# Kernel tuning notes

Hardware: AMD Instinct MI355X
Metric: run time of the kernel (lower is better)

The kernel has to match this reference:

```python
import jax, jax.numpy as jnp
import numpy as np

H, N, CH = 256, 64, 1  # heads/features, diagonal state size, channels


def setup_inputs() -> dict:
    key = jax.random.key(0)
    k1, k2, k3 = jax.random.split(key, 3)
    # |A| in (0.5, 0.999) so exp(dtA * l) decays for large l (matches rho*w construction)
    A_abslog = jnp.log(jax.random.uniform(k1, (H, N), dtype=jnp.float32,
                                          minval=0.5, maxval=0.999))
    A_phase = jax.random.uniform(k2, (H, N), dtype=jnp.float32,
                                 minval=-np.pi, maxval=np.pi)
    # C stored as real view of complex (channels, H, N, 2), like torch.view_as_real
    C = jax.random.normal(k3, (CH, H, N, 2), dtype=jnp.float32)
    return {"A_abslog": A_abslog, "A_phase": A_phase, "C": C, "L": 4096}


def reference(A_abslog, A_phase, C, L):
    # A_eigvals = exp(abslog + i*phase), copies=1 so repeat is identity
    A = jnp.exp(A_abslog + 1j * A_phase)            # (H, N) complex64
    dtA = jnp.log(A)                                 # (H, N)
    Cc = C[..., 0] + 1j * C[..., 1]                  # (CH, H, N)
    Cc = Cc * (A - 1.0) / dtA                        # (CH, H, N)
    t = jnp.arange(L, dtype=jnp.float32)             # (L,)
    K = jnp.exp(dtA[:, :, None] * t)                 # (H, N, L) Vandermonde
    K = jnp.einsum('chn,hnl->chl', Cc, K)            # (CH, H, L)
    return 2.0 * K.real
```

## Files before the change

kernel.cpp:

```cpp
#include <hip/hip_runtime.h>
#include <math.h>


typedef _Float16 f16x8 __attribute__((ext_vector_type(8)));
typedef unsigned short u16x8 __attribute__((ext_vector_type(8)));
typedef unsigned int   u32x4 __attribute__((ext_vector_type(4)));
typedef float          f32x4 __attribute__((ext_vector_type(4)));

constexpr int H = 256;
constexpr int N = 64;
constexpr int L = 4096;
constexpr int STRIDE = 76;

__global__ __launch_bounds__(256)
void sskdiag_kernel(const float* __restrict__ A_abslog,
                    const float* __restrict__ A_phase,
                    const float* __restrict__ C,
                    float* __restrict__ out)
{
    __shared__ float4   s_t1[N];
    __shared__ float4   s_t2[N];
    __shared__ unsigned s_G[64 * STRIDE];
    __shared__ unsigned s_M[64 * STRIDE];

    const int h   = blockIdx.x;
    const int tid = threadIdx.x;

    if (tid < N) {
        const int n = tid;
        const float al = A_abslog[h * N + n];
        const float ph = A_phase [h * N + n];
        const double md = (double)ph * 0.15915494309189535;
        const float phrev = (float)(md - floor(md));
        const float sp = __builtin_amdgcn_sinf(phrev);
        const float cp = __builtin_amdgcn_cosf(phrev);
        const float m  = __expf(al);
        const float Ar = m * cp, Ai = m * sp;
        const float nr = Ar - 1.0f, ni = Ai;
        const float inv = 1.0f / (al * al + ph * ph);
        const float gr = (nr * al + ni * ph) * inv;
        const float gi = (ni * al - nr * ph) * inv;
        const float cre = C[(h * N + n) * 2 + 0];
        const float cim = C[(h * N + n) * 2 + 1];
        const float Cr = 2.0f * (cre * gr - cim * gi);
        const float Ci = 2.0f * (cre * gi + cim * gr);
        const double m64 = 64.0 * md;
        const float f64a = (float)(m64 - floor(m64));
        const float mg64 = __expf(64.0f * al);
        s_t1[n] = make_float4(al, phrev, Ar, Ai);
        s_t2[n] = make_float4(mg64 * __builtin_amdgcn_cosf(f64a),
                              mg64 * __builtin_amdgcn_sinf(f64a), Cr, Ci);
    }
    __syncthreads();

    {
        const int n = tid & 63, q = tid >> 6;
        const float4 t1 = s_t1[n];
        const float4 t2 = s_t2[n];
        const float al = t1.x, phrev = t1.y;
        const float Ar = t1.z, Ai = t1.w;
        const float Ur = t2.x, Ui = t2.y;
        const float b0 = (float)(16 * q);
        float tg = phrev * b0;  tg -= floorf(tg);
        const float gmag = __expf(al * b0);
        float gre = gmag * __builtin_amdgcn_cosf(tg);
        float gim = gmag * __builtin_amdgcn_sinf(tg);
        const float a64 = (float)(1024 * q);
        float tm = phrev * a64;  tm -= floorf(tm);
        const float umag = __expf(al * a64);
        const float ure = umag * __builtin_amdgcn_cosf(tm);
        const float uim = umag * __builtin_amdgcn_sinf(tm);
        float mre = t2.z * ure - t2.w * uim;
        float mim = t2.z * uim + t2.w * ure;

        #pragma unroll
        for (int k = 0; k < 16; ++k) {
            const int row = 16 * q + k;
            union { _Float16 hh[2]; unsigned u; } pg, pm;
            pg.hh[0] = (_Float16)gre;  pg.hh[1] = (_Float16)(-gim);
            pm.hh[0] = (_Float16)mre;  pm.hh[1] = (_Float16)mim;
            s_G[row * STRIDE + n] = pg.u;
            s_M[row * STRIDE + n] = pm.u;
            const float ngr = gre * Ar - gim * Ai;
            gim = gre * Ai + gim * Ar;  gre = ngr;
            const float nmr = mre * Ur - mim * Ui;
            mim = mre * Ui + mim * Ur;  mre = nmr;
        }
    }
    __syncthreads();

    const int w    = tid >> 6;
    const int lane = tid & 63;
    const int e    = lane & 15;
    const int kg   = lane >> 4;

    f16x8 fGr[2][4], fGi[2][4], fMr[2], fMi[2];

    #pragma unroll
    for (int s = 0; s < 2; ++s) {
        #pragma unroll
        for (int tb = 0; tb < 4; ++tb) {
            const unsigned* p = &s_G[(tb * 16 + e) * STRIDE + 32 * s + 8 * kg];
            const u32x4 v0 = *reinterpret_cast<const u32x4*>(p);
            const u32x4 v1 = *reinterpret_cast<const u32x4*>(p + 4);
            u16x8 rr, ii;
            #pragma unroll
            for (int k = 0; k < 4; ++k) {
                rr[k]     = (unsigned short)(v0[k] & 0xffffu);
                ii[k]     = (unsigned short)(v0[k] >> 16);
                rr[k + 4] = (unsigned short)(v1[k] & 0xffffu);
                ii[k + 4] = (unsigned short)(v1[k] >> 16);
            }
            fGr[s][tb] = __builtin_bit_cast(f16x8, rr);
            fGi[s][tb] = __builtin_bit_cast(f16x8, ii);
        }
        {
            const unsigned* p = &s_M[(w * 16 + e) * STRIDE + 32 * s + 8 * kg];
            const u32x4 v0 = *reinterpret_cast<const u32x4*>(p);
            const u32x4 v1 = *reinterpret_cast<const u32x4*>(p + 4);
            u16x8 rr, ii;
            #pragma unroll
            for (int k = 0; k < 4; ++k) {
                rr[k]     = (unsigned short)(v0[k] & 0xffffu);
                ii[k]     = (unsigned short)(v0[k] >> 16);
                rr[k + 4] = (unsigned short)(v1[k] & 0xffffu);
                ii[k + 4] = (unsigned short)(v1[k] >> 16);
            }
            fMr[s] = __builtin_bit_cast(f16x8, rr);
            fMi[s] = __builtin_bit_cast(f16x8, ii);
        }
    }

    #pragma unroll
    for (int tb = 0; tb < 4; ++tb) {
        f32x4 acc = {0.f, 0.f, 0.f, 0.f};
        #pragma unroll
        for (int s = 0; s < 2; ++s) {
            acc = __builtin_amdgcn_mfma_f32_16x16x32_f16(fGr[s][tb], fMr[s], acc, 0, 0, 0);
            acc = __builtin_amdgcn_mfma_f32_16x16x32_f16(fGi[s][tb], fMi[s], acc, 0, 0, 0);
        }
        const int a = w * 16 + e;
        float4 v;
        v.x = acc[0];  v.y = acc[1];  v.z = acc[2];  v.w = acc[3];
        *reinterpret_cast<float4*>(out + h * L + a * 64 + tb * 16 + kg * 4) = v;
    }
}

extern "C" void kernel_launch(void* const* d_in, const int* in_sizes, int n_in,
                              void* d_out, int out_size, void* d_ws, size_t ws_size,
                              hipStream_t stream)
{
    const float* A_abslog = (const float*)d_in[0];
    const float* A_phase  = (const float*)d_in[1];
    const float* C        = (const float*)d_in[2];
    float* out = (float*)d_out;

    sskdiag_kernel<<<H, 256, 0, stream>>>(A_abslog, A_phase, C, out);
}
```

Baseline: 9.782 us.

## Split each head across four blocks to raise grid parallelism

The grid grows from one block per head to four, and each block computes a quarter of the L outputs (a 16-row slice of M) instead of all of them. Every block still recomputes the per-head setup and the full 64x64 G table. In return each wave issues fewer MFMAs and holds fewer fragments in registers. This trades repeated setup work for more blocks to fill the GPU's compute units and a smaller per-block shared-memory footprint, with a launch-bounds occupancy hint added.

```diff
diff --git a/kernel.cpp b/kernel.cpp
--- a/kernel.cpp
+++ b/kernel.cpp
@@ -2,7 +2,7 @@
 #include <math.h>
 
 
-typedef _Float16 f16x8 __attribute__((ext_vector_type(8)));
+typedef _Float16       f16x8 __attribute__((ext_vector_type(8)));
 typedef unsigned short u16x8 __attribute__((ext_vector_type(8)));
 typedef unsigned int   u32x4 __attribute__((ext_vector_type(4)));
 typedef float          f32x4 __attribute__((ext_vector_type(4)));
@@ -12,7 +12,7 @@
 constexpr int L = 4096;
 constexpr int STRIDE = 76;
 
-__global__ __launch_bounds__(256)
+__global__ __launch_bounds__(256, 4)
 void sskdiag_kernel(const float* __restrict__ A_abslog,
                     const float* __restrict__ A_phase,
                     const float* __restrict__ C,
@@ -20,10 +20,11 @@
 {
     __shared__ float4   s_t1[N];
     __shared__ float4   s_t2[N];
-    __shared__ unsigned s_G[64 * STRIDE];
-    __shared__ unsigned s_M[64 * STRIDE];
+    __shared__ __align__(16) unsigned s_G[64 * STRIDE];
+    __shared__ __align__(16) unsigned s_M[16 * STRIDE];
 
-    const int h   = blockIdx.x;
+    const int h   = blockIdx.x >> 2;
+    const int aq  = blockIdx.x & 3;
     const int tid = threadIdx.x;
 
     if (tid < N) {
@@ -60,31 +61,38 @@
         const float al = t1.x, phrev = t1.y;
         const float Ar = t1.z, Ai = t1.w;
         const float Ur = t2.x, Ui = t2.y;
-        const float b0 = (float)(16 * q);
-        float tg = phrev * b0;  tg -= floorf(tg);
-        const float gmag = __expf(al * b0);
-        float gre = gmag * __builtin_amdgcn_cosf(tg);
-        float gim = gmag * __builtin_amdgcn_sinf(tg);
-        const float a64 = (float)(1024 * q);
-        float tm = phrev * a64;  tm -= floorf(tm);
-        const float umag = __expf(al * a64);
-        const float ure = umag * __builtin_amdgcn_cosf(tm);
-        const float uim = umag * __builtin_amdgcn_sinf(tm);
-        float mre = t2.z * ure - t2.w * uim;
-        float mim = t2.z * uim + t2.w * ure;
 
-        #pragma unroll
-        for (int k = 0; k < 16; ++k) {
-            const int row = 16 * q + k;
-            union { _Float16 hh[2]; unsigned u; } pg, pm;
-            pg.hh[0] = (_Float16)gre;  pg.hh[1] = (_Float16)(-gim);
-            pm.hh[0] = (_Float16)mre;  pm.hh[1] = (_Float16)mim;
-            s_G[row * STRIDE + n] = pg.u;
-            s_M[row * STRIDE + n] = pm.u;
-            const float ngr = gre * Ar - gim * Ai;
-            gim = gre * Ai + gim * Ar;  gre = ngr;
-            const float nmr = mre * Ur - mim * Ui;
-            mim = mre * Ui + mim * Ur;  mre = nmr;
+        {
+            const float b0 = (float)(16 * q);
+            float tg = phrev * b0;  tg -= floorf(tg);
+            const float gmag = __expf(al * b0);
+            float gre = gmag * __builtin_amdgcn_cosf(tg);
+            float gim = gmag * __builtin_amdgcn_sinf(tg);
+            #pragma unroll
+            for (int k = 0; k < 16; ++k) {
+                union { _Float16 hh[2]; unsigned u; } pg;
+                pg.hh[0] = (_Float16)gre;  pg.hh[1] = (_Float16)(-gim);
+                s_G[(16 * q + k) * STRIDE + n] = pg.u;
+                const float ngr = gre * Ar - gim * Ai;
+                gim = gre * Ai + gim * Ar;  gre = ngr;
+            }
+        }
+        {
+            const float ebase = (float)(1024 * aq + 256 * q);
+            float tm = phrev * ebase;  tm -= floorf(tm);
+            const float umag = __expf(al * ebase);
+            const float ure = umag * __builtin_amdgcn_cosf(tm);
+            const float uim = umag * __builtin_amdgcn_sinf(tm);
+            float mre = t2.z * ure - t2.w * uim;
+            float mim = t2.z * uim + t2.w * ure;
+            #pragma unroll
+            for (int t = 0; t < 4; ++t) {
+                union { _Float16 hh[2]; unsigned u; } pm;
+                pm.hh[0] = (_Float16)mre;  pm.hh[1] = (_Float16)mim;
+                s_M[(4 * q + t) * STRIDE + n] = pm.u;
+                const float nmr = mre * Ur - mim * Ui;
+                mim = mre * Ui + mim * Ur;  mre = nmr;
+            }
         }
     }
     __syncthreads();
@@ -94,13 +102,12 @@
     const int e    = lane & 15;
     const int kg   = lane >> 4;
 
-    f16x8 fGr[2][4], fGi[2][4], fMr[2], fMi[2];
+    f16x8 fGr[2], fGi[2], fMr[2], fMi[2];
 
     #pragma unroll
     for (int s = 0; s < 2; ++s) {
-        #pragma unroll
-        for (int tb = 0; tb < 4; ++tb) {
-            const unsigned* p = &s_G[(tb * 16 + e) * STRIDE + 32 * s + 8 * kg];
+        {
+            const unsigned* p = &s_G[(w * 16 + e) * STRIDE + 32 * s + 8 * kg];
             const u32x4 v0 = *reinterpret_cast<const u32x4*>(p);
             const u32x4 v1 = *reinterpret_cast<const u32x4*>(p + 4);
             u16x8 rr, ii;
@@ -111,11 +118,11 @@
                 rr[k + 4] = (unsigned short)(v1[k] & 0xffffu);
                 ii[k + 4] = (unsigned short)(v1[k] >> 16);
             }
-            fGr[s][tb] = __builtin_bit_cast(f16x8, rr);
-            fGi[s][tb] = __builtin_bit_cast(f16x8, ii);
+            fGr[s] = __builtin_bit_cast(f16x8, rr);
+            fGi[s] = __builtin_bit_cast(f16x8, ii);
         }
         {
-            const unsigned* p = &s_M[(w * 16 + e) * STRIDE + 32 * s + 8 * kg];
+            const unsigned* p = &s_M[e * STRIDE + 32 * s + 8 * kg];
             const u32x4 v0 = *reinterpret_cast<const u32x4*>(p);
             const u32x4 v1 = *reinterpret_cast<const u32x4*>(p + 4);
             u16x8 rr, ii;
@@ -131,19 +138,16 @@
         }
     }
 
+    f32x4 acc = {0.f, 0.f, 0.f, 0.f};
     #pragma unroll
-    for (int tb = 0; tb < 4; ++tb) {
-        f32x4 acc = {0.f, 0.f, 0.f, 0.f};
-        #pragma unroll
-        for (int s = 0; s < 2; ++s) {
-            acc = __builtin_amdgcn_mfma_f32_16x16x32_f16(fGr[s][tb], fMr[s], acc, 0, 0, 0);
-            acc = __builtin_amdgcn_mfma_f32_16x16x32_f16(fGi[s][tb], fMi[s], acc, 0, 0, 0);
-        }
-        const int a = w * 16 + e;
-        float4 v;
-        v.x = acc[0];  v.y = acc[1];  v.z = acc[2];  v.w = acc[3];
-        *reinterpret_cast<float4*>(out + h * L + a * 64 + tb * 16 + kg * 4) = v;
+    for (int s = 0; s < 2; ++s) {
+        acc = __builtin_amdgcn_mfma_f32_16x16x32_f16(fGr[s], fMr[s], acc, 0, 0, 0);
+        acc = __builtin_amdgcn_mfma_f32_16x16x32_f16(fGi[s], fMi[s], acc, 0, 0, 0);
     }
+
+    float4 v;
+    v.x = acc[0];  v.y = acc[1];  v.z = acc[2];  v.w = acc[3];
+    *reinterpret_cast<float4*>(out + h * L + (16 * aq + e) * 64 + w * 16 + kg * 4) = v;
 }
 
 extern "C" void kernel_launch(void* const* d_in, const int* in_sizes, int n_in,
@@ -155,5 +159,5 @@
     const float* C        = (const float*)d_in[2];
     float* out = (float*)d_out;
 
-    sskdiag_kernel<<<H, 256, 0, stream>>>(A_abslog, A_phase, C, out);
+    sskdiag_kernel<<<H * 4, 256, 0, stream>>>(A_abslog, A_phase, C, out);
 }
```

After: 12.51 us. +27.9%, slower.
